# Kernel tuning notes

Hardware: AMD Instinct MI355X
Metric: run time of the kernel (lower is better)

## Reference

```python
import jax, jax.numpy as jnp
import numpy as np

T = 1000
NUM_CLASSES = 100
BATCH = 256


def setup_inputs() -> dict:
    key = jax.random.key(0)
    k_mu, k_ls, k_eps, k_y = jax.random.split(key, 4)
    mu = jax.random.normal(k_mu, (BATCH, NUM_CLASSES), dtype=jnp.float32)
    log_sigma2 = jax.random.normal(k_ls, (BATCH, NUM_CLASSES), dtype=jnp.float32)
    # MVN(0, I) samples == i.i.d. standard normals; materialized for determinism.
    eps = jax.random.normal(k_eps, (T, BATCH, NUM_CLASSES), dtype=jnp.float32)
    y = jax.random.randint(k_y, (BATCH,), 0, NUM_CLASSES, dtype=jnp.int64)
    return {"mu": mu, "log_sigma2": log_sigma2, "eps": eps, "y": y}


def reference(mu, log_sigma2, eps, y):
    t = eps.shape[0]
    log_T = jnp.asarray(np.log(t), dtype=mu.dtype)
    sigma = jnp.exp(0.5 * log_sigma2)  # [B, C]
    logits = mu[None, :, :] + sigma[None, :, :] * eps  # [T, B, C]
    # per-sample log-probabilities, weighted by 1/T in log-space
    y_hat = jax.nn.log_softmax(logits, axis=-1) - log_T  # [T, B, C]
    log_p = jax.nn.logsumexp(y_hat, axis=0)  # [B, C]
    # nll_loss with mean reduction: -mean over batch of log_p at true class
    picked = jnp.take_along_axis(log_p, y[:, None], axis=1)[:, 0]  # [B]
    return -jnp.mean(picked)
```

## Files before the change

kernel.cpp:

```cpp
#include <hip/hip_runtime.h>

#define T_TOT 1000
#define NCLS  100
#define BATCH 256
#define LOG_T 6.90775527898213705f

__global__ __launch_bounds__(256) void sigma_kernel(const float* __restrict__ ls2,
                                                    float* __restrict__ sigma) {
    int i = blockIdx.x * 256 + threadIdx.x;
    if (i < BATCH * NCLS) sigma[i] = __expf(0.5f * ls2[i]);
}

__global__ __launch_bounds__(256) void rows_kernel(const float* __restrict__ mu,
                                                   const float* __restrict__ sigma,
                                                   const float* __restrict__ eps,
                                                   const int* __restrict__ y,
                                                   float* __restrict__ v_ws) {
    const int lane = threadIdx.x & 63;
    const int half = lane >> 5;
    const int j    = lane & 31;
    const int wid  = (blockIdx.x * blockDim.x + threadIdx.x) >> 6;
    const int nw   = (gridDim.x * blockDim.x) >> 6;
    const int total_pairs = (T_TOT * BATCH) / 2;

    for (int pair = wid; pair < total_pairs; pair += nw) {
        const int r = pair * 2 + half;
        const int b = r & (BATCH - 1);
        const int t = r >> 8;

        float x0 = -INFINITY, x1 = -INFINITY, x2 = -INFINITY, x3 = -INFINITY;
        if (j < 25) {
            const float4 e4 = *(const float4*)(eps + (size_t)r * NCLS + 4 * j);
            const float4 m4 = *(const float4*)(mu  + b * NCLS + 4 * j);
            const float4 s4 = *(const float4*)(sigma + b * NCLS + 4 * j);
            x0 = fmaf(s4.x, e4.x, m4.x);
            x1 = fmaf(s4.y, e4.y, m4.y);
            x2 = fmaf(s4.z, e4.z, m4.z);
            x3 = fmaf(s4.w, e4.w, m4.w);
        }

        float m = fmaxf(fmaxf(x0, x1), fmaxf(x2, x3));
        #pragma unroll
        for (int off = 1; off <= 16; off <<= 1)
            m = fmaxf(m, __shfl_xor(m, off, 64));

        float s = __expf(x0 - m) + __expf(x1 - m) + __expf(x2 - m) + __expf(x3 - m);
        #pragma unroll
        for (int off = 1; off <= 16; off <<= 1)
            s += __shfl_xor(s, off, 64);

        const int yb = y[b];
        const int ks = yb & 3;
        const float sel = (ks == 0) ? x0 : (ks == 1) ? x1 : (ks == 2) ? x2 : x3;
        const float px = __shfl(sel, (half << 5) + (yb >> 2), 64);

        if (j == 0) v_ws[b * T_TOT + t] = px - (m + __logf(s));
    }
}

__global__ __launch_bounds__(256) void lse_kernel(const float* __restrict__ v_ws,
                                                  float* __restrict__ out) {
    const int b = blockIdx.x;
    const float* vb = v_ws + b * T_TOT;
    const int tid = threadIdx.x;

    float m = -INFINITY;
    for (int t = tid; t < T_TOT; t += 256) m = fmaxf(m, vb[t]);
    #pragma unroll
    for (int off = 1; off <= 32; off <<= 1) m = fmaxf(m, __shfl_xor(m, off, 64));

    __shared__ float red[8];
    const int wv = tid >> 6;
    if ((tid & 63) == 0) red[wv] = m;
    __syncthreads();
    m = fmaxf(fmaxf(red[0], red[1]), fmaxf(red[2], red[3]));

    float s = 0.f;
    for (int t = tid; t < T_TOT; t += 256) s += __expf(vb[t] - m);
    #pragma unroll
    for (int off = 1; off <= 32; off <<= 1) s += __shfl_xor(s, off, 64);
    if ((tid & 63) == 0) red[4 + wv] = s;
    __syncthreads();

    if (tid == 0) {
        const float ssum = red[4] + red[5] + red[6] + red[7];
        const float logp = m + __logf(ssum) - LOG_T;
        atomicAdd(out, -logp * (1.0f / BATCH));
    }
}

extern "C" void kernel_launch(void* const* d_in, const int* in_sizes, int n_in,
                              void* d_out, int out_size, void* d_ws, size_t ws_size,
                              hipStream_t stream) {
    const float* mu  = (const float*)d_in[0];
    const float* ls2 = (const float*)d_in[1];
    const float* eps = (const float*)d_in[2];
    const int*   y   = (const int*)d_in[3];
    float* out   = (float*)d_out;
    float* sigma = (float*)d_ws;
    float* v_ws  = sigma + BATCH * NCLS;

    hipMemsetAsync(out, 0, sizeof(float), stream);
    sigma_kernel<<<(BATCH * NCLS + 255) / 256, 256, 0, stream>>>(ls2, sigma);
    rows_kernel<<<2048, 256, 0, stream>>>(mu, sigma, eps, y, v_ws);
    lse_kernel<<<BATCH, 256, 0, stream>>>(v_ws, out);
}
```

Baseline: 167.0 us.

## Fuse sigma into rows kernel, hoist per-wave constants, drop max pass, single-block final reduce

The separate sigma kernel and memset are removed. Each wave now keeps a fixed batch row across its grid-stride loop, so mu, sigma (computed from log_sigma2) and y are loaded once and held in registers. The row-wise log-softmax skips the max subtraction and computes exp directly, which saves a shuffle reduction but can overflow or underflow for large logits. The final logsumexp plus mean runs in one 1024-thread block with no atomics, which cuts launches but serialises the 256 rows onto a single CU.

```diff
diff --git a/kernel.cpp b/kernel.cpp
--- a/kernel.cpp
+++ b/kernel.cpp
@@ -4,88 +4,101 @@
 #define NCLS  100
 #define BATCH 256
 #define LOG_T 6.90775527898213705f
-
-__global__ __launch_bounds__(256) void sigma_kernel(const float* __restrict__ ls2,
-                                                    float* __restrict__ sigma) {
-    int i = blockIdx.x * 256 + threadIdx.x;
-    if (i < BATCH * NCLS) sigma[i] = __expf(0.5f * ls2[i]);
-}
+#define GRID  2048
 
 __global__ __launch_bounds__(256) void rows_kernel(const float* __restrict__ mu,
-                                                   const float* __restrict__ sigma,
+                                                   const float* __restrict__ ls2,
                                                    const float* __restrict__ eps,
                                                    const int* __restrict__ y,
                                                    float* __restrict__ v_ws) {
     const int lane = threadIdx.x & 63;
     const int half = lane >> 5;
     const int j    = lane & 31;
-    const int wid  = (blockIdx.x * blockDim.x + threadIdx.x) >> 6;
-    const int nw   = (gridDim.x * blockDim.x) >> 6;
+    const int wid  = (blockIdx.x * 256 + threadIdx.x) >> 6;
+    const int nw   = (GRID * 256) >> 6;
     const int total_pairs = (T_TOT * BATCH) / 2;
+
+    const int b = (2 * wid + half) & (BATCH - 1);
+    const int yb = y[b];
+    const int ks = yb & 3;
+    const int owner = yb >> 2;
+
+    float4 m4 = make_float4(0.f, 0.f, 0.f, 0.f);
+    float4 s4 = m4;
+    if (j < 25) {
+        m4 = *(const float4*)(mu  + b * NCLS + 4 * j);
+        const float4 l4 = *(const float4*)(ls2 + b * NCLS + 4 * j);
+        s4.x = __expf(0.5f * l4.x);
+        s4.y = __expf(0.5f * l4.y);
+        s4.z = __expf(0.5f * l4.z);
+        s4.w = __expf(0.5f * l4.w);
+    }
 
     for (int pair = wid; pair < total_pairs; pair += nw) {
         const int r = pair * 2 + half;
-        const int b = r & (BATCH - 1);
         const int t = r >> 8;
 
         float x0 = -INFINITY, x1 = -INFINITY, x2 = -INFINITY, x3 = -INFINITY;
         if (j < 25) {
             const float4 e4 = *(const float4*)(eps + (size_t)r * NCLS + 4 * j);
-            const float4 m4 = *(const float4*)(mu  + b * NCLS + 4 * j);
-            const float4 s4 = *(const float4*)(sigma + b * NCLS + 4 * j);
             x0 = fmaf(s4.x, e4.x, m4.x);
             x1 = fmaf(s4.y, e4.y, m4.y);
             x2 = fmaf(s4.z, e4.z, m4.z);
             x3 = fmaf(s4.w, e4.w, m4.w);
         }
 
-        float m = fmaxf(fmaxf(x0, x1), fmaxf(x2, x3));
-        #pragma unroll
-        for (int off = 1; off <= 16; off <<= 1)
-            m = fmaxf(m, __shfl_xor(m, off, 64));
-
-        float s = __expf(x0 - m) + __expf(x1 - m) + __expf(x2 - m) + __expf(x3 - m);
+        float s = __expf(x0) + __expf(x1) + __expf(x2) + __expf(x3);
         #pragma unroll
         for (int off = 1; off <= 16; off <<= 1)
             s += __shfl_xor(s, off, 64);
 
-        const int yb = y[b];
-        const int ks = yb & 3;
-        const float sel = (ks == 0) ? x0 : (ks == 1) ? x1 : (ks == 2) ? x2 : x3;
-        const float px = __shfl(sel, (half << 5) + (yb >> 2), 64);
-
-        if (j == 0) v_ws[b * T_TOT + t] = px - (m + __logf(s));
+        if (j == owner) {
+            const float px = (ks == 0) ? x0 : (ks == 1) ? x1 : (ks == 2) ? x2 : x3;
+            v_ws[b * T_TOT + t] = px - __logf(s);
+        }
     }
 }
 
-__global__ __launch_bounds__(256) void lse_kernel(const float* __restrict__ v_ws,
-                                                  float* __restrict__ out) {
-    const int b = blockIdx.x;
-    const float* vb = v_ws + b * T_TOT;
+__global__ __launch_bounds__(1024) void lse_kernel(const float* __restrict__ v_ws,
+                                                   float* __restrict__ out) {
     const int tid = threadIdx.x;
+    const int w = tid >> 6;
+    const int l = tid & 63;
 
-    float m = -INFINITY;
-    for (int t = tid; t < T_TOT; t += 256) m = fmaxf(m, vb[t]);
-    #pragma unroll
-    for (int off = 1; off <= 32; off <<= 1) m = fmaxf(m, __shfl_xor(m, off, 64));
+    float acc = 0.f;
+    for (int b = w; b < BATCH; b += 16) {
+        const float4* vb = (const float4*)(v_ws + b * T_TOT);
+        const float4 ninf = make_float4(-INFINITY, -INFINITY, -INFINITY, -INFINITY);
+        const float4 a0 = (l       < 250) ? vb[l]       : ninf;
+        const float4 a1 = (l + 64  < 250) ? vb[l + 64]  : ninf;
+        const float4 a2 = (l + 128 < 250) ? vb[l + 128] : ninf;
+        const float4 a3 = (l + 192 < 250) ? vb[l + 192] : ninf;
 
-    __shared__ float red[8];
-    const int wv = tid >> 6;
-    if ((tid & 63) == 0) red[wv] = m;
+        float m = fmaxf(fmaxf(fmaxf(a0.x, a0.y), fmaxf(a0.z, a0.w)),
+                        fmaxf(fmaxf(a1.x, a1.y), fmaxf(a1.z, a1.w)));
+        m = fmaxf(m, fmaxf(fmaxf(fmaxf(a2.x, a2.y), fmaxf(a2.z, a2.w)),
+                           fmaxf(fmaxf(a3.x, a3.y), fmaxf(a3.z, a3.w))));
+        #pragma unroll
+        for (int off = 1; off <= 32; off <<= 1) m = fmaxf(m, __shfl_xor(m, off, 64));
+
+        float s = __expf(a0.x - m) + __expf(a0.y - m) + __expf(a0.z - m) + __expf(a0.w - m)
+                + __expf(a1.x - m) + __expf(a1.y - m) + __expf(a1.z - m) + __expf(a1.w - m)
+                + __expf(a2.x - m) + __expf(a2.y - m) + __expf(a2.z - m) + __expf(a2.w - m)
+                + __expf(a3.x - m) + __expf(a3.y - m) + __expf(a3.z - m) + __expf(a3.w - m);
+        #pragma unroll
+        for (int off = 1; off <= 32; off <<= 1) s += __shfl_xor(s, off, 64);
+
+        acc += m + __logf(s);
+    }
+
+    __shared__ float red[16];
+    if (l == 0) red[w] = acc;
     __syncthreads();
-    m = fmaxf(fmaxf(red[0], red[1]), fmaxf(red[2], red[3]));
-
-    float s = 0.f;
-    for (int t = tid; t < T_TOT; t += 256) s += __expf(vb[t] - m);
-    #pragma unroll
-    for (int off = 1; off <= 32; off <<= 1) s += __shfl_xor(s, off, 64);
-    if ((tid & 63) == 0) red[4 + wv] = s;
-    __syncthreads();
-
     if (tid == 0) {
-        const float ssum = red[4] + red[5] + red[6] + red[7];
-        const float logp = m + __logf(ssum) - LOG_T;
-        atomicAdd(out, -logp * (1.0f / BATCH));
+        float tot = 0.f;
+        #pragma unroll
+        for (int i = 0; i < 16; ++i) tot += red[i];
+        out[0] = LOG_T - tot * (1.0f / BATCH);
     }
 }
 
@@ -96,12 +109,9 @@
     const float* ls2 = (const float*)d_in[1];
     const float* eps = (const float*)d_in[2];
     const int*   y   = (const int*)d_in[3];
-    float* out   = (float*)d_out;
-    float* sigma = (float*)d_ws;
-    float* v_ws  = sigma + BATCH * NCLS;
+    float* out  = (float*)d_out;
+    float* v_ws = (float*)d_ws;
 
-    hipMemsetAsync(out, 0, sizeof(float), stream);
-    sigma_kernel<<<(BATCH * NCLS + 255) / 256, 256, 0, stream>>>(ls2, sigma);
-    rows_kernel<<<2048, 256, 0, stream>>>(mu, sigma, eps, y, v_ws);
-    lse_kernel<<<BATCH, 256, 0, stream>>>(v_ws, out);
+    rows_kernel<<<GRID, 256, 0, stream>>>(mu, ls2, eps, y, v_ws);
+    lse_kernel<<<1, 1024, 0, stream>>>(v_ws, out);
 }
```

After: 174.3 us. 1.04x slower.
